# Kernel optimization log

Hardware: AMD Instinct MI355X
Metric: run time of the kernel (lower is better)

The kernel has to match this reference:

```python
import jax, jax.numpy as jnp
import numpy as np

# irreps '128x0e + 64x1o + 32x2e' as (mul, l) pairs; ir.dim = 2*l+1
IRREPS = [(128, 0), (64, 1), (32, 2)]
B, NE = 256, 400
E_DIM, FF_DIM, HID, OUT = 32, 64, 256, 1
D = sum(m * (2 * l + 1) for m, l in IRREPS)      # 480 = irreps total dim
NCOP = sum(m for m, _ in IRREPS)                 # 224 = n_copies / inv_dim
EPS = 1e-8


def _mlp3(x, W1, b1, W2, b2, W3, b3):
    # MLP(n_layers=3): Linear+SiLU, Linear+SiLU, Linear
    h = jax.nn.silu(x @ W1 + b1)
    h = jax.nn.silu(h @ W2 + b2)
    return h @ W3 + b3


def setup_inputs() -> dict:
    key = jax.random.key(0)
    ks = jax.random.split(key, 16)

    def lin(k, i, o):
        return jax.random.normal(k, (i, o), jnp.float32) / np.float32(np.sqrt(i))

    cond_dim = E_DIM + FF_DIM            # 96
    inv_in = NCOP + FF_DIM               # 288
    return {
        "h_abs_full": jax.random.normal(ks[0], (B, D), jnp.float32),
        "e_feat": jax.random.normal(ks[1], (NE, E_DIM), jnp.float32),
        "field_abs_feat": jax.random.normal(ks[2], (B, FF_DIM), jnp.float32),
        # EnergyIrrepModulation MLP: cond_dim -> HID -> HID -> NCOP
        "mW1": lin(ks[3], cond_dim, HID), "mb1": jnp.zeros((HID,), jnp.float32),
        "mW2": lin(ks[4], HID, HID),      "mb2": jnp.zeros((HID,), jnp.float32),
        "mW3": lin(ks[5], HID, NCOP),     "mb3": jnp.zeros((NCOP,), jnp.float32),
        # out_mlp: inv_dim + ff -> HID -> HID -> OUT
        "oW1": lin(ks[6], inv_in, HID),   "ob1": jnp.zeros((HID,), jnp.float32),
        "oW2": lin(ks[7], HID, HID),      "ob2": jnp.zeros((HID,), jnp.float32),
        "oW3": lin(ks[8], HID, OUT),      "ob3": jnp.zeros((OUT,), jnp.float32),
    }


def reference(h_abs_full, e_feat, field_abs_feat,
              mW1, mb1, mW2, mb2, mW3, mb3,
              oW1, ob1, oW2, ob2, oW3, ob3):
    Bn = h_abs_full.shape[0]
    nE = e_feat.shape[0]
    ff = field_abs_feat.shape[-1]

    # cond: [B, nE, e_dim + ff]
    cond = jnp.concatenate([
        jnp.broadcast_to(e_feat[None], (Bn, nE, e_feat.shape[-1])),
        jnp.broadcast_to(field_abs_feat[:, None], (Bn, nE, ff)),
    ], axis=-1)

    # gates: [B, nE, n_copies]
    gates = _mlp3(cond, mW1, mb1, mW2, mb2, mW3, mb3)

    # Fused per-irrep broadcast gating + invariant (L2-norm) reduction.
    # h_mod[b,e, block] = x[b, block] * gate[b,e, copy]; inv = sqrt(mean(h_mod^2, dim) + eps)
    outs = []
    xoff, goff = 0, 0
    for mul, l in IRREPS:
        dim = 2 * l + 1
        xb = h_abs_full[:, xoff:xoff + mul * dim].reshape(Bn, 1, mul, dim)
        gb = gates[:, :, goff:goff + mul][..., None]          # [B, nE, mul, 1]
        m = xb * gb                                           # [B, nE, mul, dim]
        if l == 0:
            outs.append(m[..., 0])                            # scalars pass through
        else:
            outs.append(jnp.sqrt(jnp.mean(m * m, axis=-1) + EPS))
        xoff += mul * dim
        goff += mul

    inv = jnp.concatenate(
        outs + [jnp.broadcast_to(field_abs_feat[:, None], (Bn, nE, ff))], axis=-1
    )  # [B, nE, n_copies + ff]

    return _mlp3(inv, oW1, ob1, oW2, ob2, oW3, ob3)           # [B, nE, out_dim]
```

## Files before the change

### kernel.cpp

```cpp
#include <hip/hip_runtime.h>
#include <math.h>

#define BB 256
#define NE 400
#define NP (BB * NE)
#define HID 256
#define NCOP 224
#define DIN 480
#define MBLK 64
#define NBLK (NP / MBLK)

typedef _Float16 half8 __attribute__((ext_vector_type(8)));
typedef _Float16 half4 __attribute__((ext_vector_type(4)));
typedef float f4 __attribute__((ext_vector_type(4)));

static __device__ __forceinline__ float silu_f(float x) {
    float e = __builtin_amdgcn_exp2f(x * -1.44269504088896340736f);
    return x * __builtin_amdgcn_rcpf(1.0f + e);
}

static __device__ __forceinline__ int swz(int row, int colbyte) {
    return (row * 512 + colbyte) ^ ((row & 7) << 4);
}

__global__ void precompute_kernel(const float* __restrict__ h_abs,
                                  const float* __restrict__ e_feat,
                                  const float* __restrict__ field,
                                  const float* __restrict__ mW1,
                                  const float* __restrict__ mb1,
                                  const float* __restrict__ oW1,
                                  const float* __restrict__ ob1,
                                  float* __restrict__ E1,
                                  float* __restrict__ F1,
                                  float* __restrict__ Fo,
                                  float* __restrict__ S)
{
    int r = blockIdx.x;
    int t = threadIdx.x;
    if (r < NE) {
        float a = 0.f;
        #pragma unroll
        for (int k = 0; k < 32; ++k) a += e_feat[r * 32 + k] * mW1[k * HID + t];
        E1[r * HID + t] = a;
    } else if (r < NE + BB) {
        int b = r - NE;
        float a = mb1[t];
        #pragma unroll
        for (int k = 0; k < 64; ++k) a += field[b * 64 + k] * mW1[(32 + k) * HID + t];
        F1[b * HID + t] = a;
    } else if (r < NE + 2 * BB) {
        int b = r - NE - BB;
        float a = ob1[t];
        #pragma unroll
        for (int k = 0; k < 64; ++k) a += field[b * 64 + k] * oW1[(224 + k) * HID + t];
        Fo[b * HID + t] = a;
    } else {
        int b = r - NE - 2 * BB;
        if (t < 64) {
            const float* x = h_abs + b * DIN + 128 + t * 3;
            S[b * 96 + t] = (x[0]*x[0] + x[1]*x[1] + x[2]*x[2]) * (1.0f / 3.0f);
        } else if (t < 96) {
            int c = t - 64;
            const float* x = h_abs + b * DIN + 320 + c * 5;
            float s = 0.f;
            #pragma unroll
            for (int d = 0; d < 5; ++d) s += x[d] * x[d];
            S[b * 96 + t] = s * 0.2f;
        }
    }
}

__global__ void pack_weights(const float* __restrict__ mW2, const float* __restrict__ mW3,
                             const float* __restrict__ oW1, const float* __restrict__ oW2,
                             _Float16* __restrict__ PB2, _Float16* __restrict__ PB3,
                             _Float16* __restrict__ PO1, _Float16* __restrict__ PO2)
{
    int blk = blockIdx.x;
    int l = threadIdx.x;
    const float* W; _Float16* P; int LD;
    if (blk < 128)      { W = mW2; P = PB2; LD = 256; }
    else if (blk < 240) { blk -= 128; W = mW3; P = PB3; LD = 224; }
    else if (blk < 352) { blk -= 240; W = oW1; P = PO1; LD = 256; }
    else                { blk -= 352; W = oW2; P = PO2; LD = 256; }
    int KST = (P == PO1) ? 7 : 8;
    int nt = blk / KST, ks = blk - nt * KST;
    int n  = nt * 16 + (l & 15);
    int k0 = ks * 32 + (l >> 4) * 8;
    half8 v;
    #pragma unroll
    for (int j = 0; j < 8; ++j) v[j] = (_Float16)W[(size_t)(k0 + j) * LD + n];
    *(half8*)&P[(size_t)(blk * 64 + l) * 8] = v;
}

template<int KST, bool TWO>
static __device__ __forceinline__ void mma_phase(const half8* __restrict__ Wp,
                                                 const char* actp, int lane,
                                                 int tile0, f4 acc[4][2])
{
    half8 bf0[KST], bf1[TWO ? KST : 1];
    #pragma unroll
    for (int ks = 0; ks < KST; ++ks)
        bf0[ks] = Wp[(tile0 * KST + ks) * 64 + lane];
    if (TWO) {
        #pragma unroll
        for (int ks = 0; ks < KST; ++ks)
            bf1[ks] = Wp[((tile0 + 8) * KST + ks) * 64 + lane];
    }

    #pragma unroll
    for (int mt = 0; mt < 4; ++mt) {
        acc[mt][0] = (f4){0.f, 0.f, 0.f, 0.f};
        acc[mt][1] = (f4){0.f, 0.f, 0.f, 0.f};
    }

    #pragma unroll
    for (int ks = 0; ks < KST; ++ks) {
        int kb = ks * 64 + ((lane >> 4) << 4);
        half8 a[4];
        #pragma unroll
        for (int mt = 0; mt < 4; ++mt) {
            int row = mt * 16 + (lane & 15);
            a[mt] = *(const half8*)(actp + ((row * 512 + kb) ^ ((row & 7) << 4)));
        }
        #pragma unroll
        for (int mt = 0; mt < 4; ++mt)
            acc[mt][0] = __builtin_amdgcn_mfma_f32_16x16x32_f16(bf0[ks], a[mt], acc[mt][0], 0, 0, 0);
        if (TWO) {
            #pragma unroll
            for (int mt = 0; mt < 4; ++mt)
                acc[mt][1] = __builtin_amdgcn_mfma_f32_16x16x32_f16(bf1[ks], a[mt], acc[mt][1], 0, 0, 0);
        }
    }
}

__global__ __launch_bounds__(512, 1)
void fused_mfma(const float* __restrict__ h_abs,
                const float* __restrict__ mb2, const float* __restrict__ mb3,
                const float* __restrict__ ob2,
                const float* __restrict__ oW3, const float* __restrict__ ob3,
                const float* __restrict__ E1, const float* __restrict__ F1,
                const float* __restrict__ Fo, const float* __restrict__ S,
                const half8* __restrict__ PB2, const half8* __restrict__ PB3,
                const half8* __restrict__ PO1, const half8* __restrict__ PO2,
                float* __restrict__ out)
{
    __shared__ char act[MBLK * 512];
    __shared__ float sred[8][64];

    const int t    = threadIdx.x;
    const int lane = t & 63;
    const int w    = t >> 6;
    const int p0   = blockIdx.x * MBLK;
    const int lr   = lane & 15;
    const int lq   = lane >> 4;

    const int b0 = p0 / NE;
    const int r0 = p0 - b0 * NE;

    {
        #pragma unroll
        for (int i = 0; i < 4; ++i) {
            int c   = i * 512 + t;
            int row = c >> 5;
            int c0  = (c & 31) * 8;
            int e = r0 + row;
            int b = b0;
            if (e >= NE) { e -= NE; b += 1; }
            const f4* ep = (const f4*)&E1[e * HID + c0];
            const f4* fp = (const f4*)&F1[b * HID + c0];
            f4 e0 = ep[0], e1 = ep[1];
            f4 f0 = fp[0], f1 = fp[1];
            half8 hv;
            #pragma unroll
            for (int j = 0; j < 4; ++j) hv[j]     = (_Float16)silu_f(e0[j] + f0[j]);
            #pragma unroll
            for (int j = 0; j < 4; ++j) hv[4 + j] = (_Float16)silu_f(e1[j] + f1[j]);
            *(half8*)(act + swz(row, c0 * 2)) = hv;
        }
    }
    __syncthreads();

    f4 acc[4][2];

    mma_phase<8, true>(PB2, act, lane, w, acc);
    __syncthreads();
    #pragma unroll
    for (int ntj = 0; ntj < 2; ++ntj) {
        int n0 = (w + ntj * 8) * 16 + lq * 4;
        f4 bias = *(const f4*)&mb2[n0];
        #pragma unroll
        for (int mt = 0; mt < 4; ++mt) {
            int row = mt * 16 + lr;
            half4 hv;
            #pragma unroll
            for (int r = 0; r < 4; ++r)
                hv[r] = (_Float16)silu_f(acc[mt][ntj][r] + bias[r]);
            *(half4*)(act + swz(row, n0 * 2)) = hv;
        }
    }
    __syncthreads();

    if (w < 6) mma_phase<8, true >(PB3, act, lane, w, acc);
    else       mma_phase<8, false>(PB3, act, lane, w, acc);
    __syncthreads();
    #pragma unroll
    for (int ntj = 0; ntj < 2; ++ntj) {
        int tile = w + ntj * 8;
        if (tile < 14) {
            int n0 = tile * 16 + lq * 4;
            f4 bias = *(const f4*)&mb3[n0];
            #pragma unroll
            for (int mt = 0; mt < 4; ++mt) {
                int row = mt * 16 + lr;
                int b = b0 + ((r0 + row) >= NE);
                half4 hv;
                if (n0 < 128) {
                    f4 xh = *(const f4*)&h_abs[b * DIN + n0];
                    #pragma unroll
                    for (int r = 0; r < 4; ++r)
                        hv[r] = (_Float16)(xh[r] * (acc[mt][ntj][r] + bias[r]));
                } else {
                    f4 sv = *(const f4*)&S[b * 96 + (n0 - 128)];
                    #pragma unroll
                    for (int r = 0; r < 4; ++r) {
                        float g = acc[mt][ntj][r] + bias[r];
                        hv[r] = (_Float16)__builtin_amdgcn_sqrtf(g * g * sv[r] + 1e-8f);
                    }
                }
                *(half4*)(act + swz(row, n0 * 2)) = hv;
            }
        }
    }
    __syncthreads();

    mma_phase<7, true>(PO1, act, lane, w, acc);
    __syncthreads();
    #pragma unroll
    for (int ntj = 0; ntj < 2; ++ntj) {
        int n0 = (w + ntj * 8) * 16 + lq * 4;
        #pragma unroll
        for (int mt = 0; mt < 4; ++mt) {
            int row = mt * 16 + lr;
            int b = b0 + ((r0 + row) >= NE);
            f4 fo = *(const f4*)&Fo[b * HID + n0];
            half4 hv;
            #pragma unroll
            for (int r = 0; r < 4; ++r)
                hv[r] = (_Float16)silu_f(acc[mt][ntj][r] + fo[r]);
            *(half4*)(act + swz(row, n0 * 2)) = hv;
        }
    }
    __syncthreads();

    mma_phase<8, true>(PO2, act, lane, w, acc);
    {
        float partial[4] = {0.f, 0.f, 0.f, 0.f};
        #pragma unroll
        for (int ntj = 0; ntj < 2; ++ntj) {
            int n0 = (w + ntj * 8) * 16 + lq * 4;
            f4 bias = *(const f4*)&ob2[n0];
            f4 wv   = *(const f4*)&oW3[n0];
            #pragma unroll
            for (int mt = 0; mt < 4; ++mt)
                #pragma unroll
                for (int r = 0; r < 4; ++r)
                    partial[mt] += silu_f(acc[mt][ntj][r] + bias[r]) * wv[r];
        }
        #pragma unroll
        for (int mt = 0; mt < 4; ++mt) {
            float s = partial[mt];
            s += __shfl_xor(s, 16, 64);
            s += __shfl_xor(s, 32, 64);
            if (lq == 0) sred[w][mt * 16 + lr] = s;
        }
    }
    __syncthreads();
    if (t < 64) {
        float s = ob3[0];
        #pragma unroll
        for (int ww = 0; ww < 8; ++ww) s += sred[ww][t];
        out[p0 + t] = s;
    }
}

extern "C" void kernel_launch(void* const* d_in, const int* in_sizes, int n_in,
                              void* d_out, int out_size, void* d_ws, size_t ws_size,
                              hipStream_t stream) {
    const float* h_abs  = (const float*)d_in[0];
    const float* e_feat = (const float*)d_in[1];
    const float* field  = (const float*)d_in[2];
    const float* mW1 = (const float*)d_in[3];
    const float* mb1 = (const float*)d_in[4];
    const float* mW2 = (const float*)d_in[5];
    const float* mb2 = (const float*)d_in[6];
    const float* mW3 = (const float*)d_in[7];
    const float* mb3 = (const float*)d_in[8];
    const float* oW1 = (const float*)d_in[9];
    const float* ob1 = (const float*)d_in[10];
    const float* oW2 = (const float*)d_in[11];
    const float* ob2 = (const float*)d_in[12];
    const float* oW3 = (const float*)d_in[13];
    const float* ob3 = (const float*)d_in[14];
    float* out = (float*)d_out;

    float* ws = (float*)d_ws;
    float* E1 = ws;
    float* F1 = E1 + NE * HID;
    float* Fo = F1 + BB * HID;
    float* S  = Fo + BB * HID;
    _Float16* PB2 = (_Float16*)(S + BB * 96);
    _Float16* PB3 = PB2 + 16 * 8 * 64 * 8;
    _Float16* PO1 = PB3 + 14 * 8 * 64 * 8;
    _Float16* PO2 = PO1 + 16 * 7 * 64 * 8;

    precompute_kernel<<<NE + 3 * BB, 256, 0, stream>>>(
        h_abs, e_feat, field, mW1, mb1, oW1, ob1, E1, F1, Fo, S);

    pack_weights<<<480, 64, 0, stream>>>(
        mW2, mW3, oW1, oW2, PB2, PB3, PO1, PO2);

    fused_mfma<<<NBLK, 512, 0, stream>>>(
        h_abs, mb2, mb3, ob2, oW3, ob3,
        E1, F1, Fo, S,
        (const half8*)PB2, (const half8*)PB3, (const half8*)PO1, (const half8*)PO2,
        out);
}
```

Baseline: 99.13 us.

## Prefetch next layer weight fragments and epilogue operands during current MFMA phase

Splits the MFMA phase into fragment loading and compute so each layer's packed weight fragments are issued before the preceding compute or barrier, overlapping global load latency with the previous layer's work. Epilogue operands (h_abs, S, Fo) are also loaded into registers ahead of the barrier instead of inside the epilogue loops. This raises register pressure (extra fragment arrays live across phases at 512 threads, launch bounds 1), which may cause spills or limit scheduling.

```diff
diff --git a/kernel.cpp b/kernel.cpp
--- a/kernel.cpp
+++ b/kernel.cpp
@@ -93,26 +93,30 @@
 }
 
 template<int KST, bool TWO>
-static __device__ __forceinline__ void mma_phase(const half8* __restrict__ Wp,
-                                                 const char* actp, int lane,
-                                                 int tile0, f4 acc[4][2])
-{
-    half8 bf0[KST], bf1[TWO ? KST : 1];
+static __device__ __forceinline__ void load_frags(const half8* __restrict__ Wp,
+                                                  int lane, int tile0,
+                                                  half8 f0[], half8 f1[])
+{
     #pragma unroll
     for (int ks = 0; ks < KST; ++ks)
-        bf0[ks] = Wp[(tile0 * KST + ks) * 64 + lane];
+        f0[ks] = Wp[(tile0 * KST + ks) * 64 + lane];
     if (TWO) {
         #pragma unroll
         for (int ks = 0; ks < KST; ++ks)
-            bf1[ks] = Wp[((tile0 + 8) * KST + ks) * 64 + lane];
-    }
-
+            f1[ks] = Wp[((tile0 + 8) * KST + ks) * 64 + lane];
+    }
+}
+
+template<int KST, bool TWO>
+static __device__ __forceinline__ void mma_compute(const half8 f0[], const half8 f1[],
+                                                   const char* actp, int lane,
+                                                   f4 acc[4][2])
+{
     #pragma unroll
     for (int mt = 0; mt < 4; ++mt) {
         acc[mt][0] = (f4){0.f, 0.f, 0.f, 0.f};
         acc[mt][1] = (f4){0.f, 0.f, 0.f, 0.f};
     }
-
     #pragma unroll
     for (int ks = 0; ks < KST; ++ks) {
         int kb = ks * 64 + ((lane >> 4) << 4);
@@ -124,11 +128,11 @@
         }
         #pragma unroll
         for (int mt = 0; mt < 4; ++mt)
-            acc[mt][0] = __builtin_amdgcn_mfma_f32_16x16x32_f16(bf0[ks], a[mt], acc[mt][0], 0, 0, 0);
+            acc[mt][0] = __builtin_amdgcn_mfma_f32_16x16x32_f16(f0[ks], a[mt], acc[mt][0], 0, 0, 0);
         if (TWO) {
             #pragma unroll
             for (int mt = 0; mt < 4; ++mt)
-                acc[mt][1] = __builtin_amdgcn_mfma_f32_16x16x32_f16(bf1[ks], a[mt], acc[mt][1], 0, 0, 0);
+                acc[mt][1] = __builtin_amdgcn_mfma_f32_16x16x32_f16(f1[ks], a[mt], acc[mt][1], 0, 0, 0);
         }
     }
 }
@@ -156,6 +160,9 @@
 
     const int b0 = p0 / NE;
     const int r0 = p0 - b0 * NE;
+
+    half8 fb0[8], fb1[8];
+    load_frags<8, true>(PB2, lane, w, fb0, fb1);
 
     {
         #pragma unroll
@@ -182,7 +189,10 @@
 
     f4 acc[4][2];
 
-    mma_phase<8, true>(PB2, act, lane, w, acc);
+    mma_compute<8, true>(fb0, fb1, act, lane, acc);
+    half8 fc0[8], fc1[8];
+    if (w < 6) load_frags<8, true >(PB3, lane, w, fc0, fc1);
+    else       load_frags<8, false>(PB3, lane, w, fc0, fc1);
     __syncthreads();
     #pragma unroll
     for (int ntj = 0; ntj < 2; ++ntj) {
@@ -200,40 +210,66 @@
     }
     __syncthreads();
 
-    if (w < 6) mma_phase<8, true >(PB3, act, lane, w, acc);
-    else       mma_phase<8, false>(PB3, act, lane, w, acc);
-    __syncthreads();
-    #pragma unroll
-    for (int ntj = 0; ntj < 2; ++ntj) {
-        int tile = w + ntj * 8;
-        if (tile < 14) {
-            int n0 = tile * 16 + lq * 4;
-            f4 bias = *(const f4*)&mb3[n0];
+    if (w < 6) mma_compute<8, true >(fc0, fc1, act, lane, acc);
+    else       mma_compute<8, false>(fc0, fc1, act, lane, acc);
+    half8 fd0[7], fd1[7];
+    load_frags<7, true>(PO1, lane, w, fd0, fd1);
+    int bmt[4];
+    #pragma unroll
+    for (int mt = 0; mt < 4; ++mt)
+        bmt[mt] = b0 + ((r0 + mt * 16 + lr) >= NE);
+    f4 xh[4], sv[4];
+    {
+        int nc = w * 16 + lq * 4;
+        #pragma unroll
+        for (int mt = 0; mt < 4; ++mt)
+            xh[mt] = *(const f4*)&h_abs[bmt[mt] * DIN + nc];
+        if (w < 6) {
+            #pragma unroll
+            for (int mt = 0; mt < 4; ++mt)
+                sv[mt] = *(const f4*)&S[bmt[mt] * 96 + nc];
+        }
+    }
+    __syncthreads();
+    {
+        int n0 = w * 16 + lq * 4;
+        f4 bias = *(const f4*)&mb3[n0];
+        #pragma unroll
+        for (int mt = 0; mt < 4; ++mt) {
+            int row = mt * 16 + lr;
+            half4 hv;
+            #pragma unroll
+            for (int r = 0; r < 4; ++r)
+                hv[r] = (_Float16)(xh[mt][r] * (acc[mt][0][r] + bias[r]));
+            *(half4*)(act + swz(row, n0 * 2)) = hv;
+        }
+        if (w < 6) {
+            int n1 = (w + 8) * 16 + lq * 4;
+            f4 bias1 = *(const f4*)&mb3[n1];
             #pragma unroll
             for (int mt = 0; mt < 4; ++mt) {
                 int row = mt * 16 + lr;
-                int b = b0 + ((r0 + row) >= NE);
                 half4 hv;
-                if (n0 < 128) {
-                    f4 xh = *(const f4*)&h_abs[b * DIN + n0];
-                    #pragma unroll
-                    for (int r = 0; r < 4; ++r)
-                        hv[r] = (_Float16)(xh[r] * (acc[mt][ntj][r] + bias[r]));
-                } else {
-                    f4 sv = *(const f4*)&S[b * 96 + (n0 - 128)];
-                    #pragma unroll
-                    for (int r = 0; r < 4; ++r) {
-                        float g = acc[mt][ntj][r] + bias[r];
-                        hv[r] = (_Float16)__builtin_amdgcn_sqrtf(g * g * sv[r] + 1e-8f);
-                    }
+                #pragma unroll
+                for (int r = 0; r < 4; ++r) {
+                    float g = acc[mt][1][r] + bias1[r];
+                    hv[r] = (_Float16)__builtin_amdgcn_sqrtf(g * g * sv[mt][r] + 1e-8f);
                 }
-                *(half4*)(act + swz(row, n0 * 2)) = hv;
+                *(half4*)(act + swz(row, n1 * 2)) = hv;
             }
         }
     }
     __syncthreads();
 
-    mma_phase<7, true>(PO1, act, lane, w, acc);
+    mma_compute<7, true>(fd0, fd1, act, lane, acc);
+    half8 fe0[8], fe1[8];
+    load_frags<8, true>(PO2, lane, w, fe0, fe1);
+    f4 fo[4][2];
+    #pragma unroll
+    for (int mt = 0; mt < 4; ++mt)
+        #pragma unroll
+        for (int ntj = 0; ntj < 2; ++ntj)
+            fo[mt][ntj] = *(const f4*)&Fo[bmt[mt] * HID + (w + ntj * 8) * 16 + lq * 4];
     __syncthreads();
     #pragma unroll
     for (int ntj = 0; ntj < 2; ++ntj) {
@@ -241,18 +277,16 @@
         #pragma unroll
         for (int mt = 0; mt < 4; ++mt) {
             int row = mt * 16 + lr;
-            int b = b0 + ((r0 + row) >= NE);
-            f4 fo = *(const f4*)&Fo[b * HID + n0];
             half4 hv;
             #pragma unroll
             for (int r = 0; r < 4; ++r)
-                hv[r] = (_Float16)silu_f(acc[mt][ntj][r] + fo[r]);
+                hv[r] = (_Float16)silu_f(acc[mt][ntj][r] + fo[mt][ntj][r]);
             *(half4*)(act + swz(row, n0 * 2)) = hv;
         }
     }
     __syncthreads();
 
-    mma_phase<8, true>(PO2, act, lane, w, acc);
+    mma_compute<8, true>(fe0, fe1, act, lane, acc);
     {
         float partial[4] = {0.f, 0.f, 0.f, 0.f};
         #pragma unroll
```

Result: slower. 101.3 us (+2.2%).

## Retile MFMA phases to 2x4 warp grid and fold biases into accumulators

Applied to the files above, without the earlier changes.

Each of the 8 waves now covers 32 rows by 4 column tiles, arranged as a 2x4 grid, instead of all 64 rows by 2 tiles. This halves the per-wave LDS activation reads and doubles the register-resident weight fragments. Biases and the Fo term now initialize the accumulators instead of being added in the epilogue. The h_abs and S loads for the gating stage are issued before the barrier so they overlap the MFMA work. The cost is higher register pressure, since each wave holds 32 weight fragments, which may spill.

```diff
diff --git a/kernel.cpp b/kernel.cpp
--- a/kernel.cpp
+++ b/kernel.cpp
@@ -92,44 +92,32 @@
     *(half8*)&P[(size_t)(blk * 64 + l) * 8] = v;
 }
 
-template<int KST, bool TWO>
-static __device__ __forceinline__ void mma_phase(const half8* __restrict__ Wp,
-                                                 const char* actp, int lane,
-                                                 int tile0, f4 acc[4][2])
+template<int KST, int NT>
+static __device__ __forceinline__ void mma_phase4(const half8* __restrict__ Wp,
+                                                  const char* actp, int lane,
+                                                  int wh, int wc, f4 acc[4][2])
 {
-    half8 bf0[KST], bf1[TWO ? KST : 1];
-    #pragma unroll
-    for (int ks = 0; ks < KST; ++ks)
-        bf0[ks] = Wp[(tile0 * KST + ks) * 64 + lane];
-    if (TWO) {
+    half8 bf[NT][KST];
+    #pragma unroll
+    for (int ti = 0; ti < NT; ++ti)
         #pragma unroll
         for (int ks = 0; ks < KST; ++ks)
-            bf1[ks] = Wp[((tile0 + 8) * KST + ks) * 64 + lane];
-    }
-
-    #pragma unroll
-    for (int mt = 0; mt < 4; ++mt) {
-        acc[mt][0] = (f4){0.f, 0.f, 0.f, 0.f};
-        acc[mt][1] = (f4){0.f, 0.f, 0.f, 0.f};
-    }
+            bf[ti][ks] = Wp[((wc + ti * 4) * KST + ks) * 64 + lane];
 
     #pragma unroll
     for (int ks = 0; ks < KST; ++ks) {
         int kb = ks * 64 + ((lane >> 4) << 4);
-        half8 a[4];
-        #pragma unroll
-        for (int mt = 0; mt < 4; ++mt) {
-            int row = mt * 16 + (lane & 15);
+        half8 a[2];
+        #pragma unroll
+        for (int mt = 0; mt < 2; ++mt) {
+            int row = wh * 32 + mt * 16 + (lane & 15);
             a[mt] = *(const half8*)(actp + ((row * 512 + kb) ^ ((row & 7) << 4)));
         }
         #pragma unroll
-        for (int mt = 0; mt < 4; ++mt)
-            acc[mt][0] = __builtin_amdgcn_mfma_f32_16x16x32_f16(bf0[ks], a[mt], acc[mt][0], 0, 0, 0);
-        if (TWO) {
-            #pragma unroll
-            for (int mt = 0; mt < 4; ++mt)
-                acc[mt][1] = __builtin_amdgcn_mfma_f32_16x16x32_f16(bf1[ks], a[mt], acc[mt][1], 0, 0, 0);
-        }
+        for (int ti = 0; ti < NT; ++ti)
+            #pragma unroll
+            for (int mt = 0; mt < 2; ++mt)
+                acc[ti][mt] = __builtin_amdgcn_mfma_f32_16x16x32_f16(bf[ti][ks], a[mt], acc[ti][mt], 0, 0, 0);
     }
 }
 
@@ -145,17 +133,23 @@
                 float* __restrict__ out)
 {
     __shared__ char act[MBLK * 512];
-    __shared__ float sred[8][64];
+    __shared__ float sred[4][64];
 
     const int t    = threadIdx.x;
     const int lane = t & 63;
     const int w    = t >> 6;
+    const int wh   = w & 1;
+    const int wc   = w >> 1;
     const int p0   = blockIdx.x * MBLK;
     const int lr   = lane & 15;
     const int lq   = lane >> 4;
 
     const int b0 = p0 / NE;
     const int r0 = p0 - b0 * NE;
+
+    int nt_[4];
+    #pragma unroll
+    for (int ti = 0; ti < 4; ++ti) nt_[ti] = (wc + ti * 4) * 16 + lq * 4;
 
     {
         #pragma unroll
@@ -182,103 +176,141 @@
 
     f4 acc[4][2];
 
-    mma_phase<8, true>(PB2, act, lane, w, acc);
-    __syncthreads();
-    #pragma unroll
-    for (int ntj = 0; ntj < 2; ++ntj) {
-        int n0 = (w + ntj * 8) * 16 + lq * 4;
-        f4 bias = *(const f4*)&mb2[n0];
-        #pragma unroll
-        for (int mt = 0; mt < 4; ++mt) {
-            int row = mt * 16 + lr;
+    #pragma unroll
+    for (int ti = 0; ti < 4; ++ti) {
+        f4 bb = *(const f4*)&mb2[nt_[ti]];
+        acc[ti][0] = bb; acc[ti][1] = bb;
+    }
+    mma_phase4<8, 4>(PB2, act, lane, wh, wc, acc);
+    __syncthreads();
+    #pragma unroll
+    for (int ti = 0; ti < 4; ++ti)
+        #pragma unroll
+        for (int mt = 0; mt < 2; ++mt) {
+            int row = wh * 32 + mt * 16 + lr;
             half4 hv;
             #pragma unroll
             for (int r = 0; r < 4; ++r)
-                hv[r] = (_Float16)silu_f(acc[mt][ntj][r] + bias[r]);
-            *(half4*)(act + swz(row, n0 * 2)) = hv;
-        }
-    }
-    __syncthreads();
-
-    if (w < 6) mma_phase<8, true >(PB3, act, lane, w, acc);
-    else       mma_phase<8, false>(PB3, act, lane, w, acc);
-    __syncthreads();
-    #pragma unroll
-    for (int ntj = 0; ntj < 2; ++ntj) {
-        int tile = w + ntj * 8;
-        if (tile < 14) {
-            int n0 = tile * 16 + lq * 4;
-            f4 bias = *(const f4*)&mb3[n0];
-            #pragma unroll
-            for (int mt = 0; mt < 4; ++mt) {
-                int row = mt * 16 + lr;
-                int b = b0 + ((r0 + row) >= NE);
+                hv[r] = (_Float16)silu_f(acc[ti][mt][r]);
+            *(half4*)(act + swz(row, nt_[ti] * 2)) = hv;
+        }
+    __syncthreads();
+
+    #pragma unroll
+    for (int ti = 0; ti < 4; ++ti) {
+        f4 bb = (ti < 3 || wc < 2) ? *(const f4*)&mb3[nt_[ti]] : (f4){0.f,0.f,0.f,0.f};
+        acc[ti][0] = bb; acc[ti][1] = bb;
+    }
+    if (wc < 2) mma_phase4<8, 4>(PB3, act, lane, wh, wc, acc);
+    else        mma_phase4<8, 3>(PB3, act, lane, wh, wc, acc);
+    int bmt[2];
+    #pragma unroll
+    for (int mt = 0; mt < 2; ++mt)
+        bmt[mt] = b0 + ((r0 + wh * 32 + mt * 16 + lr) >= NE);
+    f4 xh[2][2], sv0[2], sv1[2];
+    #pragma unroll
+    for (int ti = 0; ti < 2; ++ti)
+        #pragma unroll
+        for (int mt = 0; mt < 2; ++mt)
+            xh[ti][mt] = *(const f4*)&h_abs[bmt[mt] * DIN + nt_[ti]];
+    #pragma unroll
+    for (int mt = 0; mt < 2; ++mt)
+        sv0[mt] = *(const f4*)&S[bmt[mt] * 96 + nt_[0]];
+    if (wc < 2) {
+        #pragma unroll
+        for (int mt = 0; mt < 2; ++mt)
+            sv1[mt] = *(const f4*)&S[bmt[mt] * 96 + nt_[1]];
+    }
+    __syncthreads();
+    {
+        #pragma unroll
+        for (int ti = 0; ti < 2; ++ti)
+            #pragma unroll
+            for (int mt = 0; mt < 2; ++mt) {
+                int row = wh * 32 + mt * 16 + lr;
                 half4 hv;
-                if (n0 < 128) {
-                    f4 xh = *(const f4*)&h_abs[b * DIN + n0];
-                    #pragma unroll
-                    for (int r = 0; r < 4; ++r)
-                        hv[r] = (_Float16)(xh[r] * (acc[mt][ntj][r] + bias[r]));
-                } else {
-                    f4 sv = *(const f4*)&S[b * 96 + (n0 - 128)];
-                    #pragma unroll
-                    for (int r = 0; r < 4; ++r) {
-                        float g = acc[mt][ntj][r] + bias[r];
-                        hv[r] = (_Float16)__builtin_amdgcn_sqrtf(g * g * sv[r] + 1e-8f);
-                    }
-                }
-                *(half4*)(act + swz(row, n0 * 2)) = hv;
-            }
-        }
-    }
-    __syncthreads();
-
-    mma_phase<7, true>(PO1, act, lane, w, acc);
-    __syncthreads();
-    #pragma unroll
-    for (int ntj = 0; ntj < 2; ++ntj) {
-        int n0 = (w + ntj * 8) * 16 + lq * 4;
-        #pragma unroll
-        for (int mt = 0; mt < 4; ++mt) {
-            int row = mt * 16 + lr;
-            int b = b0 + ((r0 + row) >= NE);
-            f4 fo = *(const f4*)&Fo[b * HID + n0];
-            half4 hv;
-            #pragma unroll
-            for (int r = 0; r < 4; ++r)
-                hv[r] = (_Float16)silu_f(acc[mt][ntj][r] + fo[r]);
-            *(half4*)(act + swz(row, n0 * 2)) = hv;
-        }
-    }
-    __syncthreads();
-
-    mma_phase<8, true>(PO2, act, lane, w, acc);
-    {
-        float partial[4] = {0.f, 0.f, 0.f, 0.f};
-        #pragma unroll
-        for (int ntj = 0; ntj < 2; ++ntj) {
-            int n0 = (w + ntj * 8) * 16 + lq * 4;
-            f4 bias = *(const f4*)&ob2[n0];
-            f4 wv   = *(const f4*)&oW3[n0];
-            #pragma unroll
-            for (int mt = 0; mt < 4; ++mt)
                 #pragma unroll
                 for (int r = 0; r < 4; ++r)
-                    partial[mt] += silu_f(acc[mt][ntj][r] + bias[r]) * wv[r];
-        }
-        #pragma unroll
-        for (int mt = 0; mt < 4; ++mt) {
+                    hv[r] = (_Float16)(xh[ti][mt][r] * acc[ti][mt][r]);
+                *(half4*)(act + swz(row, nt_[ti] * 2)) = hv;
+            }
+        #pragma unroll
+        for (int mt = 0; mt < 2; ++mt) {
+            int row = wh * 32 + mt * 16 + lr;
+            half4 hv;
+            #pragma unroll
+            for (int r = 0; r < 4; ++r) {
+                float g = acc[2][mt][r];
+                hv[r] = (_Float16)__builtin_amdgcn_sqrtf(g * g * sv0[mt][r] + 1e-8f);
+            }
+            *(half4*)(act + swz(row, nt_[2] * 2)) = hv;
+        }
+        if (wc < 2) {
+            #pragma unroll
+            for (int mt = 0; mt < 2; ++mt) {
+                int row = wh * 32 + mt * 16 + lr;
+                half4 hv;
+                #pragma unroll
+                for (int r = 0; r < 4; ++r) {
+                    float g = acc[3][mt][r];
+                    hv[r] = (_Float16)__builtin_amdgcn_sqrtf(g * g * sv1[mt][r] + 1e-8f);
+                }
+                *(half4*)(act + swz(row, nt_[3] * 2)) = hv;
+            }
+        }
+    }
+    __syncthreads();
+
+    #pragma unroll
+    for (int ti = 0; ti < 4; ++ti)
+        #pragma unroll
+        for (int mt = 0; mt < 2; ++mt)
+            acc[ti][mt] = *(const f4*)&Fo[bmt[mt] * HID + nt_[ti]];
+    mma_phase4<7, 4>(PO1, act, lane, wh, wc, acc);
+    __syncthreads();
+    #pragma unroll
+    for (int ti = 0; ti < 4; ++ti)
+        #pragma unroll
+        for (int mt = 0; mt < 2; ++mt) {
+            int row = wh * 32 + mt * 16 + lr;
+            half4 hv;
+            #pragma unroll
+            for (int r = 0; r < 4; ++r)
+                hv[r] = (_Float16)silu_f(acc[ti][mt][r]);
+            *(half4*)(act + swz(row, nt_[ti] * 2)) = hv;
+        }
+    __syncthreads();
+
+    #pragma unroll
+    for (int ti = 0; ti < 4; ++ti) {
+        f4 bb = *(const f4*)&ob2[nt_[ti]];
+        acc[ti][0] = bb; acc[ti][1] = bb;
+    }
+    mma_phase4<8, 4>(PO2, act, lane, wh, wc, acc);
+    {
+        float partial[2] = {0.f, 0.f};
+        #pragma unroll
+        for (int ti = 0; ti < 4; ++ti) {
+            f4 wv = *(const f4*)&oW3[nt_[ti]];
+            #pragma unroll
+            for (int mt = 0; mt < 2; ++mt)
+                #pragma unroll
+                for (int r = 0; r < 4; ++r)
+                    partial[mt] += silu_f(acc[ti][mt][r]) * wv[r];
+        }
+        #pragma unroll
+        for (int mt = 0; mt < 2; ++mt) {
             float s = partial[mt];
             s += __shfl_xor(s, 16, 64);
             s += __shfl_xor(s, 32, 64);
-            if (lq == 0) sred[w][mt * 16 + lr] = s;
+            if (lq == 0) sred[wc][wh * 32 + mt * 16 + lr] = s;
         }
     }
     __syncthreads();
     if (t < 64) {
         float s = ob3[0];
         #pragma unroll
-        for (int ww = 0; ww < 8; ++ww) s += sred[ww][t];
+        for (int cc = 0; cc < 4; ++cc) s += sred[cc][t];
         out[p0 + t] = s;
     }
 }
```

Result: slower. 131.8 us (+32.9%).
